# Performance work log

Hardware: AMD Instinct MI355X
Metric: run time of the kernel (lower is better)

## Reference

```python
import jax, jax.numpy as jnp
import numpy as np

C = 64          # channels
K = 15          # sum(shell_sizes)=1+14
H = 32          # neighbors per query
N = 50000       # support points (== query points M)
RADIUS = 1.0
SIGMA = 0.7
INF = 1e6
BN_EPS = 1e-5


def _init_kernel_points(key):
    # stand-in for load_kernels: 1 center point + 14 points on a sphere shell
    pts = jax.random.normal(key, (K - 1, 3), dtype=jnp.float32)
    pts = pts / jnp.linalg.norm(pts, axis=1, keepdims=True) * RADIUS
    return jnp.concatenate([jnp.zeros((1, 3), jnp.float32), pts], axis=0)


def setup_inputs() -> dict:
    key = jax.random.key(0)
    ks = jax.random.split(key, 10)
    q_pts = jax.random.normal(ks[0], (N, 3), dtype=jnp.float32)
    s_pts = jax.random.normal(ks[1], (N, 3), dtype=jnp.float32)
    s_feats = jax.random.normal(ks[2], (N, C), dtype=jnp.float32)
    neighb_inds = jax.random.randint(ks[3], (N, H), 0, N)
    kernel_points = _init_kernel_points(ks[4])
    # alpha_mlp: Linear(C->C, no bias) -> BatchNorm -> LeakyReLU(0.1) -> Linear(C->K*C)
    lim1 = 1.0 / np.sqrt(C)
    W1 = jax.random.uniform(ks[5], (C, C), jnp.float32, -lim1, lim1)
    gamma = jnp.ones((C,), jnp.float32)
    beta = jnp.zeros((C,), jnp.float32)
    W2 = jax.random.uniform(ks[6], (C, K * C), jnp.float32, -lim1, lim1)
    b2 = jax.random.uniform(ks[7], (K * C,), jnp.float32, -lim1, lim1)
    return {"q_pts": q_pts, "s_pts": s_pts, "s_feats": s_feats,
            "neighb_inds": neighb_inds, "kernel_points": kernel_points,
            "W1": W1, "gamma": gamma, "beta": beta, "W2": W2, "b2": b2}


def reference(q_pts, s_pts, s_feats, neighb_inds, kernel_points, W1, gamma, beta, W2, b2):
    M = q_pts.shape[0]
    # alpha_mlp on pooled (= center) features: (M, C) -> (M, K*C)
    h = s_feats @ W1
    mu = jnp.mean(h, axis=0)
    var = jnp.var(h, axis=0)
    h = (h - mu) / jnp.sqrt(var + BN_EPS) * gamma + beta
    h = jax.nn.leaky_relu(h, 0.1)
    conv_weights = (h @ W2 + b2).reshape(M, K, C)

    # gather neighbor features with a zero padding row (index N -> zeros)
    padded_feats = jnp.concatenate([s_feats, jnp.zeros((1, C), s_feats.dtype)], axis=0)
    neighbor_feats = padded_feats[neighb_inds]                 # (M, H, C)

    # relative neighbor positions with inf padding point
    s_pts_pad = jnp.concatenate([s_pts, jnp.full((1, 3), INF, s_pts.dtype)], axis=0)
    neighbors = s_pts_pad[neighb_inds] - q_pts[:, None, :]     # (M, H, 3)

    # kernel-point influence: nearest kernel point + linear influence
    diff = neighbors[:, :, None, :] - kernel_points            # (M, H, K, 3)
    sq_d = jnp.sum(diff * diff, axis=-1)                       # (M, H, K)
    nn_sq = jnp.min(sq_d, axis=-1)                             # (M, H)
    nn_idx = jnp.argmin(sq_d, axis=-1)                         # (M, H)
    infl = jnp.clip(1.0 - jnp.sqrt(nn_sq) / SIGMA, 0.0)        # (M, H)

    # per-neighbor channel weights from the MLP output, gathered by 1nn kernel point
    nw = jnp.take_along_axis(conv_weights, nn_idx[:, :, None], axis=1)  # (M, H, C)
    nw = nw * infl[:, :, None]

    # weighted aggregation (merge=mul, aggr=sum over neighbors)
    return jnp.sum(neighbor_feats * nw, axis=1)                # (M, C)
```

## Files before the change

### kernel.cpp

```cpp
#include <hip/hip_runtime.h>
#include <math.h>

#define N_PTS 50000
#define CCH   64
#define KP    15
#define NH    32
#define SIGMA 0.7f
#define BN_EPS 1e-5f
#define LEAKY 0.1f
#define QB    16
#define STATS_BLOCKS 1024
#define CW_KSTRIDE_B 2176

typedef short bf16x8 __attribute__((ext_vector_type(8)));
typedef float floatx4 __attribute__((ext_vector_type(4)));

__device__ __forceinline__ unsigned short f2b(float f) {
    union { float f; unsigned u; } v; v.f = f;
    return (unsigned short)((v.u + 0x7FFFu + ((v.u >> 16) & 1u)) >> 16);
}
__device__ __forceinline__ float b2f(unsigned short b) {
    union { unsigned u; float f; } v; v.u = ((unsigned)b) << 16;
    return v.f;
}
__device__ __forceinline__ float blo(unsigned u) {
    union { unsigned u; float f; } v; v.u = u << 16;
    return v.f;
}
__device__ __forceinline__ float bhi(unsigned u) {
    union { unsigned u; float f; } v; v.u = u & 0xFFFF0000u;
    return v.f;
}

__global__ __launch_bounds__(256) void k_prep(const float* __restrict__ sf,
                                              const float* __restrict__ W1,
                                              const float* __restrict__ W2,
                                              float* __restrict__ bn,
                                              unsigned short* __restrict__ hst,
                                              unsigned short* __restrict__ w2b,
                                              unsigned short* __restrict__ sfb) {
    int t = threadIdx.x;
    if (blockIdx.x >= STATS_BLOCKS) {
        int g = (blockIdx.x - STATS_BLOCKS) * 256 + t;
        int lane = g & 63, s = (g >> 6) & 1, tt = g >> 7;
        int col = lane & 15, quad = lane >> 4;
        int base = (s * 32 + quad * 8) * 960 + tt * 16 + col;
        ushort4 lo, hi;
        lo.x = f2b(W2[base + 0 * 960]); lo.y = f2b(W2[base + 1 * 960]);
        lo.z = f2b(W2[base + 2 * 960]); lo.w = f2b(W2[base + 3 * 960]);
        hi.x = f2b(W2[base + 4 * 960]); hi.y = f2b(W2[base + 5 * 960]);
        hi.z = f2b(W2[base + 6 * 960]); hi.w = f2b(W2[base + 7 * 960]);
        *(ushort4*)(w2b + g * 8)     = lo;
        *(ushort4*)(w2b + g * 8 + 4) = hi;
        return;
    }
    int c = t & 63, ml = t >> 6;
    float w1c[64];
    #pragma unroll
    for (int i = 0; i < 64; ++i) w1c[i] = W1[i * 64 + c];
    __shared__ float rows[4][64];
    float acc_s = 0.f, acc_q = 0.f;
    for (int m0 = blockIdx.x * 4; m0 < N_PTS; m0 += STATS_BLOCKS * 4) {
        __syncthreads();
        float v = sf[m0 * 64 + t];
        ((float*)rows)[t] = v;
        sfb[m0 * 64 + t] = f2b(v);
        __syncthreads();
        float h = 0.f;
        #pragma unroll
        for (int i4 = 0; i4 < 16; ++i4) {
            float4 r = *(const float4*)&rows[ml][i4 * 4];
            h += r.x * w1c[i4 * 4] + r.y * w1c[i4 * 4 + 1]
               + r.z * w1c[i4 * 4 + 2] + r.w * w1c[i4 * 4 + 3];
        }
        acc_s += h;
        acc_q += h * h;
        hst[(m0 + ml) * 64 + c] = f2b(h);
    }
    __shared__ float red[2][256];
    red[0][t] = acc_s; red[1][t] = acc_q;
    __syncthreads();
    if (t < 64) {
        float s = red[0][t] + red[0][64 + t] + red[0][128 + t] + red[0][192 + t];
        float q = red[1][t] + red[1][64 + t] + red[1][128 + t] + red[1][192 + t];
        atomicAdd(&bn[t], s);
        atomicAdd(&bn[64 + t], q);
    }
}

__global__ __launch_bounds__(256, 4) void k_main(
    const float* __restrict__ q_pts, const float* __restrict__ s_pts,
    const unsigned short* __restrict__ sfb, const int* __restrict__ nb,
    const float* __restrict__ kpts, const float* __restrict__ gamma,
    const float* __restrict__ beta, const float* __restrict__ bn,
    const float* __restrict__ b2, const unsigned short* __restrict__ w2b,
    const unsigned short* __restrict__ hst, float* __restrict__ out) {

    __shared__ __align__(16) unsigned cwP[KP * 32 * 17];
    __shared__ float abS[128];
    __shared__ int      nCnt[QB];
    __shared__ unsigned nPack[QB][NH];
    __shared__ float    nInf[QB][NH];

    int t = threadIdx.x;
    int lane = t & 63, wv = t >> 6;
    int m0 = blockIdx.x * QB;

    if (t < 64) {
        float mu  = bn[t] * (1.0f / N_PTS);
        float var = bn[64 + t] * (1.0f / N_PTS) - mu * mu;
        float a   = gamma[t] * rsqrtf(var + BN_EPS);
        abS[t]      = a;
        abS[64 + t] = beta[t] - mu * a;
    } else if (t >= 64 && t < 64 + QB) {
        nCnt[t - 64] = 0;
    }
    ((unsigned*)nPack)[t]       = 0u;
    ((unsigned*)nPack)[t + 256] = 0u;
    ((float*)nInf)[t]           = 0.f;
    ((float*)nInf)[t + 256]     = 0.f;
    __syncthreads();

    int row = lane & 15, half = lane >> 4;
    bf16x8 a0, a1;
    {
        const unsigned short* hrow = hst + (m0 + row) * 64 + half * 8;
        bf16x8 r0 = *(const bf16x8*)(hrow);
        bf16x8 r1 = *(const bf16x8*)(hrow + 32);
        #pragma unroll
        for (int j = 0; j < 8; ++j) {
            int c0 = half * 8 + j;
            float g0 = abS[c0] * b2f((unsigned short)r0[j]) + abS[64 + c0];
            g0 = g0 > 0.f ? g0 : LEAKY * g0;
            a0[j] = (short)f2b(g0);
            int c1 = 32 + c0;
            float g1 = abS[c1] * b2f((unsigned short)r1[j]) + abS[64 + c1];
            g1 = g1 > 0.f ? g1 : LEAKY * g1;
            a1[j] = (short)f2b(g1);
        }
    }

    {
        int q = lane & 15, quad = lane >> 4;
        #pragma unroll 3
        for (int ti = 0; ti < 15; ++ti) {
            int tt = wv * 15 + ti;
            bf16x8 bf0 = *(const bf16x8*)(w2b + ((tt * 2 + 0) * 64 + lane) * 8);
            bf16x8 bf1 = *(const bf16x8*)(w2b + ((tt * 2 + 1) * 64 + lane) * 8);
            floatx4 acc = {0.f, 0.f, 0.f, 0.f};
            acc = __builtin_amdgcn_mfma_f32_16x16x32_bf16(bf0, a0, acc, 0, 0, 0);
            acc = __builtin_amdgcn_mfma_f32_16x16x32_bf16(bf1, a1, acc, 0, 0, 0);
            int n0 = tt * 16 + quad * 4;
            float4 bb = *(const float4*)&b2[n0];
            int k  = n0 >> 6;
            int c2 = (n0 & 63) >> 1;
            unsigned w0 = (unsigned)f2b(acc[0] + bb.x) | ((unsigned)f2b(acc[1] + bb.y) << 16);
            unsigned w1 = (unsigned)f2b(acc[2] + bb.z) | ((unsigned)f2b(acc[3] + bb.w) << 16);
            unsigned* dst = cwP + (k * 544 + c2 * 17 + q);
            dst[0]  = w0;
            dst[17] = w1;
        }
    }

    float kpr[45];
    #pragma unroll
    for (int i = 0; i < 45; ++i) kpr[i] = kpts[i];

    for (int task = t; task < QB * NH; task += 256) {
        int q = task >> 5, hh = task & 31;
        int m = m0 + q;
        int idx = nb[m * NH + hh];
        float px = s_pts[idx * 3 + 0] - q_pts[m * 3 + 0];
        float py = s_pts[idx * 3 + 1] - q_pts[m * 3 + 1];
        float pz = s_pts[idx * 3 + 2] - q_pts[m * 3 + 2];
        float best = 1e30f; int bi = 0;
        #pragma unroll
        for (int k = 0; k < KP; ++k) {
            float dx = px - kpr[k * 3], dy = py - kpr[k * 3 + 1], dz = pz - kpr[k * 3 + 2];
            float d = dx * dx + dy * dy + dz * dz;
            if (d < best) { best = d; bi = k; }
        }
        float infl = 1.f - sqrtf(best) * (1.0f / SIGMA);
        if (infl > 0.f) {
            int pos = atomicAdd(&nCnt[q], 1);
            nPack[q][pos] = (unsigned)idx | ((unsigned)(bi * CW_KSTRIDE_B) << 16);
            nInf[q][pos]  = infl;
        }
    }
    __syncthreads();

    {
        int r = lane >> 5, c2 = lane & 31;
        const unsigned short* sfbC = sfb + c2 * 2;
        const unsigned char* cwB = (const unsigned char*)cwP;
        #pragma unroll
        for (int pp = 0; pp < 2; ++pp) {
            int qa = wv * 4 + pp * 2;
            int q  = qa + r;
            const unsigned* packRow = &nPack[q][0];
            const float*    infRow  = &nInf[q][0];
            const unsigned char* cwLane = cwB + (c2 * 17 + q) * 4;
            int nA = nCnt[qa], nB = nCnt[qa + 1];
            int na = nA > nB ? nA : nB;
            float acc0 = 0.f, acc1 = 0.f;
            for (int jj = 0; jj < na; jj += 4) {
                uint4  pk = *(const uint4*)&packRow[jj];
                float4 in = *(const float4*)&infRow[jj];
                unsigned f0 = *(const unsigned*)(sfbC + (pk.x & 0xFFFFu) * 64);
                unsigned f1 = *(const unsigned*)(sfbC + (pk.y & 0xFFFFu) * 64);
                unsigned f2 = *(const unsigned*)(sfbC + (pk.z & 0xFFFFu) * 64);
                unsigned f3 = *(const unsigned*)(sfbC + (pk.w & 0xFFFFu) * 64);
                unsigned w0 = *(const unsigned*)(cwLane + (pk.x >> 16));
                unsigned w1 = *(const unsigned*)(cwLane + (pk.y >> 16));
                unsigned w2 = *(const unsigned*)(cwLane + (pk.z >> 16));
                unsigned w3 = *(const unsigned*)(cwLane + (pk.w >> 16));
                acc0 = fmaf(in.x * blo(f0), blo(w0), acc0);
                acc1 = fmaf(in.x * bhi(f0), bhi(w0), acc1);
                acc0 = fmaf(in.y * blo(f1), blo(w1), acc0);
                acc1 = fmaf(in.y * bhi(f1), bhi(w1), acc1);
                acc0 = fmaf(in.z * blo(f2), blo(w2), acc0);
                acc1 = fmaf(in.z * bhi(f2), bhi(w2), acc1);
                acc0 = fmaf(in.w * blo(f3), blo(w3), acc0);
                acc1 = fmaf(in.w * bhi(f3), bhi(w3), acc1);
            }
            float2 o; o.x = acc0; o.y = acc1;
            *(float2*)&out[(m0 + q) * 64 + c2 * 2] = o;
        }
    }
}

extern "C" void kernel_launch(void* const* d_in, const int* in_sizes, int n_in,
                              void* d_out, int out_size, void* d_ws, size_t ws_size,
                              hipStream_t stream) {
    const float* q_pts   = (const float*)d_in[0];
    const float* s_pts   = (const float*)d_in[1];
    const float* s_feats = (const float*)d_in[2];
    const int*   nb      = (const int*)d_in[3];
    const float* kpts    = (const float*)d_in[4];
    const float* W1      = (const float*)d_in[5];
    const float* gamma   = (const float*)d_in[6];
    const float* beta    = (const float*)d_in[7];
    const float* W2      = (const float*)d_in[8];
    const float* b2      = (const float*)d_in[9];
    float* out = (float*)d_out;

    float* ws = (float*)d_ws;
    float* bn = ws;
    unsigned short* w2b = (unsigned short*)(ws + 128);
    unsigned short* hst = w2b + 61440;
    unsigned short* sfb = hst + N_PTS * CCH;

    hipMemsetAsync(bn, 0, 128 * sizeof(float), stream);
    k_prep<<<STATS_BLOCKS + 30, 256, 0, stream>>>(s_feats, W1, W2, bn, hst, w2b, sfb);
    k_main<<<N_PTS / QB, 256, 0, stream>>>(q_pts, s_pts, sfb, nb, kpts,
                                           gamma, beta, bn, b2, w2b, hst, out);
}
```

Measured before the change: 159.3 us.

## Reorder conv-weight MFMA after neighbor scan, prefetch W2 tiles, use ballot compaction

The neighbor influence scan now runs before the per-block MLP matmul, so the gather latency of neighbor indices and positions can overlap with the later MFMA work. The W2 bf16 fragments are double-buffered in registers in groups of three tiles. Shared-memory atomic counters are replaced by wave ballot and popcount compaction, which relies on each 32-lane half-wave mapping to exactly one query. Float-to-bf16 packing uses the hardware v_cvt_pk_bf16_f32 instruction instead of manual rounding, at the cost of more live registers.

```diff
diff --git a/kernel.cpp b/kernel.cpp
--- a/kernel.cpp
+++ b/kernel.cpp
@@ -30,6 +30,11 @@
 __device__ __forceinline__ float bhi(unsigned u) {
     union { unsigned u; float f; } v; v.u = u & 0xFFFF0000u;
     return v.f;
+}
+__device__ __forceinline__ unsigned cvtpk(float lo, float hi) {
+    unsigned r;
+    asm("v_cvt_pk_bf16_f32 %0, %1, %2" : "=v"(r) : "v"(lo), "v"(hi));
+    return r;
 }
 
 __global__ __launch_bounds__(256) void k_prep(const float* __restrict__ sf,
@@ -112,8 +117,6 @@
         float a   = gamma[t] * rsqrtf(var + BN_EPS);
         abS[t]      = a;
         abS[64 + t] = beta[t] - mu * a;
-    } else if (t >= 64 && t < 64 + QB) {
-        nCnt[t - 64] = 0;
     }
     ((unsigned*)nPack)[t]       = 0u;
     ((unsigned*)nPack)[t + 256] = 0u;
@@ -122,51 +125,20 @@
     __syncthreads();
 
     int row = lane & 15, half = lane >> 4;
-    bf16x8 a0, a1;
+    bf16x8 r0, r1;
     {
         const unsigned short* hrow = hst + (m0 + row) * 64 + half * 8;
-        bf16x8 r0 = *(const bf16x8*)(hrow);
-        bf16x8 r1 = *(const bf16x8*)(hrow + 32);
-        #pragma unroll
-        for (int j = 0; j < 8; ++j) {
-            int c0 = half * 8 + j;
-            float g0 = abS[c0] * b2f((unsigned short)r0[j]) + abS[64 + c0];
-            g0 = g0 > 0.f ? g0 : LEAKY * g0;
-            a0[j] = (short)f2b(g0);
-            int c1 = 32 + c0;
-            float g1 = abS[c1] * b2f((unsigned short)r1[j]) + abS[64 + c1];
-            g1 = g1 > 0.f ? g1 : LEAKY * g1;
-            a1[j] = (short)f2b(g1);
-        }
-    }
-
-    {
-        int q = lane & 15, quad = lane >> 4;
-        #pragma unroll 3
-        for (int ti = 0; ti < 15; ++ti) {
-            int tt = wv * 15 + ti;
-            bf16x8 bf0 = *(const bf16x8*)(w2b + ((tt * 2 + 0) * 64 + lane) * 8);
-            bf16x8 bf1 = *(const bf16x8*)(w2b + ((tt * 2 + 1) * 64 + lane) * 8);
-            floatx4 acc = {0.f, 0.f, 0.f, 0.f};
-            acc = __builtin_amdgcn_mfma_f32_16x16x32_bf16(bf0, a0, acc, 0, 0, 0);
-            acc = __builtin_amdgcn_mfma_f32_16x16x32_bf16(bf1, a1, acc, 0, 0, 0);
-            int n0 = tt * 16 + quad * 4;
-            float4 bb = *(const float4*)&b2[n0];
-            int k  = n0 >> 6;
-            int c2 = (n0 & 63) >> 1;
-            unsigned w0 = (unsigned)f2b(acc[0] + bb.x) | ((unsigned)f2b(acc[1] + bb.y) << 16);
-            unsigned w1 = (unsigned)f2b(acc[2] + bb.z) | ((unsigned)f2b(acc[3] + bb.w) << 16);
-            unsigned* dst = cwP + (k * 544 + c2 * 17 + q);
-            dst[0]  = w0;
-            dst[17] = w1;
-        }
+        r0 = *(const bf16x8*)(hrow);
+        r1 = *(const bf16x8*)(hrow + 32);
     }
 
     float kpr[45];
     #pragma unroll
     for (int i = 0; i < 45; ++i) kpr[i] = kpts[i];
 
-    for (int task = t; task < QB * NH; task += 256) {
+    #pragma unroll
+    for (int it = 0; it < 2; ++it) {
+        int task = t + 256 * it;
         int q = task >> 5, hh = task & 31;
         int m = m0 + q;
         int idx = nb[m * NH + hh];
@@ -181,10 +153,77 @@
             if (d < best) { best = d; bi = k; }
         }
         float infl = 1.f - sqrtf(best) * (1.0f / SIGMA);
-        if (infl > 0.f) {
-            int pos = atomicAdd(&nCnt[q], 1);
+        bool keep = infl > 0.f;
+        unsigned long long bal = __ballot(keep);
+        unsigned mym = (unsigned)(bal >> (lane & 32));
+        int pos = __popc(mym & ((1u << (lane & 31)) - 1u));
+        if (keep) {
             nPack[q][pos] = (unsigned)idx | ((unsigned)(bi * CW_KSTRIDE_B) << 16);
             nInf[q][pos]  = infl;
+        }
+        if ((lane & 31) == 0) nCnt[q] = __popc(mym);
+    }
+
+    bf16x8 a0, a1;
+    {
+        unsigned* A0 = (unsigned*)&a0;
+        unsigned* A1 = (unsigned*)&a1;
+        #pragma unroll
+        for (int jw = 0; jw < 4; ++jw) {
+            int c0 = half * 8 + jw * 2;
+            float g00 = abS[c0]     * b2f((unsigned short)r0[jw * 2])     + abS[64 + c0];
+            float g01 = abS[c0 + 1] * b2f((unsigned short)r0[jw * 2 + 1]) + abS[64 + c0 + 1];
+            g00 = g00 > 0.f ? g00 : LEAKY * g00;
+            g01 = g01 > 0.f ? g01 : LEAKY * g01;
+            A0[jw] = cvtpk(g00, g01);
+            int c1 = 32 + c0;
+            float g10 = abS[c1]     * b2f((unsigned short)r1[jw * 2])     + abS[64 + c1];
+            float g11 = abS[c1 + 1] * b2f((unsigned short)r1[jw * 2 + 1]) + abS[64 + c1 + 1];
+            g10 = g10 > 0.f ? g10 : LEAKY * g10;
+            g11 = g11 > 0.f ? g11 : LEAKY * g11;
+            A1[jw] = cvtpk(g10, g11);
+        }
+    }
+
+    {
+        int colq = lane & 15, quad = lane >> 4;
+        bf16x8 Lf[3], Ls[3], Mf[3], Ms[3];
+        #pragma unroll
+        for (int i = 0; i < 3; ++i) {
+            int tt = wv * 15 + i;
+            Lf[i] = *(const bf16x8*)(w2b + ((tt * 2 + 0) * 64 + lane) * 8);
+            Ls[i] = *(const bf16x8*)(w2b + ((tt * 2 + 1) * 64 + lane) * 8);
+        }
+        #pragma unroll
+        for (int g = 0; g < 5; ++g) {
+            if (g < 4) {
+                #pragma unroll
+                for (int i = 0; i < 3; ++i) {
+                    int tt = wv * 15 + (g + 1) * 3 + i;
+                    Mf[i] = *(const bf16x8*)(w2b + ((tt * 2 + 0) * 64 + lane) * 8);
+                    Ms[i] = *(const bf16x8*)(w2b + ((tt * 2 + 1) * 64 + lane) * 8);
+                }
+            }
+            #pragma unroll
+            for (int i = 0; i < 3; ++i) {
+                int tt = wv * 15 + g * 3 + i;
+                floatx4 acc = {0.f, 0.f, 0.f, 0.f};
+                acc = __builtin_amdgcn_mfma_f32_16x16x32_bf16(Lf[i], a0, acc, 0, 0, 0);
+                acc = __builtin_amdgcn_mfma_f32_16x16x32_bf16(Ls[i], a1, acc, 0, 0, 0);
+                int n0 = tt * 16 + quad * 4;
+                float4 bb = *(const float4*)&b2[n0];
+                int k  = n0 >> 6;
+                int c2 = (n0 & 63) >> 1;
+                unsigned w0 = cvtpk(acc[0] + bb.x, acc[1] + bb.y);
+                unsigned w1 = cvtpk(acc[2] + bb.z, acc[3] + bb.w);
+                unsigned* dst = cwP + (k * 544 + c2 * 17 + colq);
+                dst[0]  = w0;
+                dst[17] = w1;
+            }
+            if (g < 4) {
+                #pragma unroll
+                for (int i = 0; i < 3; ++i) { Lf[i] = Mf[i]; Ls[i] = Ms[i]; }
+            }
         }
     }
     __syncthreads();
```

After: 156.4 us. About the same (-1.8%).
